# Kernel tuning notes

Measured on AMD Instinct MI355X. Metric: run time of the kernel, lower is better.

## Reference

```python
import jax, jax.numpy as jnp
import numpy as np

N, E = 50000, 800000
ND, ED, H, L = 128, 32, 128, 4


def _mlp2(x, w1, b1, w2, b2):
    return jax.nn.relu(x @ w1 + b1) @ w2 + b2


def _layer_norm(x, g, b, eps=1e-5):
    m = jnp.mean(x, axis=-1, keepdims=True)
    v = jnp.var(x, axis=-1, keepdims=True)
    return (x - m) * jax.lax.rsqrt(v + eps) * g + b


def setup_inputs() -> dict:
    key = jax.random.key(0)
    ks = iter(jax.random.split(key, 40))
    r = lambda *s: jax.random.normal(next(ks), s, jnp.float32) * 0.05
    return dict(
        x=r(N, ND),
        edge_attr=r(E, ED),
        h_prev=r(N, H),
        enc_w1=r(ND, H), enc_b1=jnp.zeros((H,), jnp.float32),
        enc_w2=r(H, H), enc_b2=jnp.zeros((H,), jnp.float32),
        et_w1=r(L, 2 * H + ED, H), et_b1=jnp.zeros((L, H), jnp.float32),
        et_w2=r(L, H, H), et_b2=jnp.zeros((L, H), jnp.float32),
        msg_w1=r(L, H, H), msg_b1=jnp.zeros((L, H), jnp.float32),
        msg_w2=r(L, H, H), msg_b2=jnp.zeros((L, H), jnp.float32),
        upd_w1=r(L, 2 * H, H), upd_b1=jnp.zeros((L, H), jnp.float32),
        upd_w2=r(L, H, H), upd_b2=jnp.zeros((L, H), jnp.float32),
        ln_g=jnp.ones((H,), jnp.float32), ln_b=jnp.zeros((H,), jnp.float32),
        gru_wih=r(3 * H, H), gru_whh=r(3 * H, H),
        gru_bih=jnp.zeros((3 * H,), jnp.float32),
        gru_bhh=jnp.zeros((3 * H,), jnp.float32),
        edge_index=jax.random.randint(next(ks), (2, E), 0, N, jnp.int32),
    )


def reference(x, edge_attr, h_prev,
              enc_w1, enc_b1, enc_w2, enc_b2,
              et_w1, et_b1, et_w2, et_b2,
              msg_w1, msg_b1, msg_w2, msg_b2,
              upd_w1, upd_b1, upd_w2, upd_b2,
              ln_g, ln_b,
              gru_wih, gru_whh, gru_bih, gru_bhh,
              edge_index):
    src, dst = edge_index[0], edge_index[1]  # PyG: x_j = x[src], x_i = x[dst]
    n_nodes = x.shape[0]
    h = _mlp2(x, enc_w1, enc_b1, enc_w2, enc_b2)  # [N, H]
    for l in range(et_w1.shape[0]):
        x_i = h[dst]                                  # [E, H] gather (target)
        x_j = h[src]                                  # [E, H] gather (source)
        e_in = jnp.concatenate([x_i, x_j, edge_attr], axis=-1)  # [E, 2H+ED]
        e_emb = _mlp2(e_in, et_w1[l], et_b1[l], et_w2[l], et_b2[l])
        msg = _mlp2(e_emb, msg_w1[l], msg_b1[l], msg_w2[l], msg_b2[l])
        aggr = jax.ops.segment_sum(msg, dst, num_segments=n_nodes)  # [N, H]
        h_new = _mlp2(jnp.concatenate([h, aggr], axis=-1),
                      upd_w1[l], upd_b1[l], upd_w2[l], upd_b2[l])
        h = _layer_norm(h + h_new, ln_g, ln_b)
    # GRUCell(input=h, hidden=h_prev), torch semantics
    gi = h @ gru_wih.T + gru_bih          # [N, 3H]
    gh = h_prev @ gru_whh.T + gru_bhh     # [N, 3H]
    i_r, i_z, i_n = jnp.split(gi, 3, axis=-1)
    h_r, h_z, h_n = jnp.split(gh, 3, axis=-1)
    r = jax.nn.sigmoid(i_r + h_r)
    z = jax.nn.sigmoid(i_z + h_z)
    n = jnp.tanh(i_n + r * h_n)
    return (1.0 - z) * n + z * h_prev
```

## Files before the change

kernel.cpp:

```cpp
#include <hip/hip_runtime.h>
#include <hip/hip_bf16.h>
#include <cstdint>

#define NN 50000
#define NE 800000

typedef _Float16 f16;
typedef f16 f16x8 __attribute__((ext_vector_type(8)));
typedef f16 f16x4 __attribute__((ext_vector_type(4)));
typedef float f32x4 __attribute__((ext_vector_type(4)));

#define TB_STR 136

__global__ void hist_kernel(const int* __restrict__ edst, int* __restrict__ deg) {
  int e = blockIdx.x * 256 + threadIdx.x;
  if (e < NE) atomicAdd(&deg[edst[e]], 1);
}

__global__ void scan_kernel(const int* __restrict__ deg, int* __restrict__ offs, int n) {
  __shared__ int tmp[256];
  __shared__ int carry;
  const int tid = threadIdx.x;
  if (tid == 0) carry = 0;
  __syncthreads();
  for (int base = 0; base < n; base += 1024) {
    int v[4]; int s = 0;
#pragma unroll
    for (int j = 0; j < 4; ++j) {
      int idx = base + tid * 4 + j;
      v[j] = (idx < n) ? deg[idx] : 0;
      s += v[j];
    }
    tmp[tid] = s;
    __syncthreads();
    for (int ofs = 1; ofs < 256; ofs <<= 1) {
      int t = (tid >= ofs) ? tmp[tid - ofs] : 0;
      __syncthreads();
      tmp[tid] += t;
      __syncthreads();
    }
    int excl = carry + tmp[tid] - s;
#pragma unroll
    for (int j = 0; j < 4; ++j) {
      int idx = base + tid * 4 + j;
      if (idx < n) offs[idx] = excl;
      excl += v[j];
    }
    __syncthreads();
    if (tid == 255) carry += tmp[255];
    __syncthreads();
  }
  if (tid == 0) offs[n] = carry;
}

__global__ void copy_cursor_kernel(const int* __restrict__ offs, int* __restrict__ cursor) {
  int i = blockIdx.x * 256 + threadIdx.x;
  if (i < NN) cursor[i] = offs[i];
}

__global__ void fill_kernel(const int* __restrict__ edst, int* __restrict__ cursor,
                            int* __restrict__ eord) {
  int e = blockIdx.x * 256 + threadIdx.x;
  if (e < NE) {
    int p = atomicAdd(&cursor[edst[e]], 1);
    eord[p] = e;
  }
}

__global__ void permute_kernel(const int* __restrict__ eord,
                               const int* __restrict__ esrc,
                               const int* __restrict__ edst,
                               const float* __restrict__ ea,
                               int* __restrict__ dstp, int* __restrict__ esp,
                               f16* __restrict__ ea16p) {
  int i = blockIdx.x * 256 + threadIdx.x;
  if (i >= NE) return;
  int e = eord[i];
  dstp[i] = edst[e];
  esp[i] = esrc[e];
  const float* sp = ea + (size_t)e * 32;
  f16* dp = ea16p + (size_t)i * 32;
#pragma unroll
  for (int j = 0; j < 4; ++j) {
    float4 u0 = *(const float4*)(sp + j * 8), u1 = *(const float4*)(sp + j * 8 + 4);
    f16x8 v = {(f16)u0.x, (f16)u0.y, (f16)u0.z, (f16)u0.w,
               (f16)u1.x, (f16)u1.y, (f16)u1.z, (f16)u1.w};
    *(f16x8*)(dp + j * 8) = v;
  }
}

__global__ void w23_kernel(const float* __restrict__ et_w2,
                           const float* __restrict__ et_b2,
                           const float* __restrict__ msg_w1,
                           const float* __restrict__ msg_b1,
                           float* __restrict__ w23, float* __restrict__ b23) {
  const int l = blockIdx.x >> 3, cc = blockIdx.x & 7;
  const float* W2 = et_w2 + (size_t)l * 16384;
  const float* W3 = msg_w1 + (size_t)l * 16384;
  __shared__ float w3s[128][17];
  const int tid = threadIdx.x;
#pragma unroll
  for (int it = 0; it < 8; ++it) {
    int f = tid + it * 256;
    int m = f >> 4, n = f & 15;
    w3s[m][n] = W3[m * 128 + cc * 16 + n];
  }
  __syncthreads();
  const int k = tid >> 1, nh = (tid & 1) * 8;
  float s[8] = {};
  for (int m = 0; m < 128; ++m) {
    float w2v = W2[k * 128 + m];
#pragma unroll
    for (int j = 0; j < 8; ++j) s[j] = fmaf(w2v, w3s[m][nh + j], s[j]);
  }
#pragma unroll
  for (int j = 0; j < 8; ++j)
    w23[(size_t)l * 16384 + k * 128 + cc * 16 + nh + j] = s[j];
  if (k == 0) {
    float sb[8] = {};
    for (int m = 0; m < 128; ++m) {
      float b2v = et_b2[l * 128 + m];
#pragma unroll
      for (int j = 0; j < 8; ++j) sb[j] = fmaf(b2v, w3s[m][nh + j], sb[j]);
    }
#pragma unroll
    for (int j = 0; j < 8; ++j)
      b23[l * 128 + cc * 16 + nh + j] = sb[j] + msg_b1[l * 128 + cc * 16 + nh + j];
  }
}

__global__ void pack_w_kernel(const float* __restrict__ et_w1,
                              const float* __restrict__ w23,
                              const float* __restrict__ msg_w2,
                              f16* __restrict__ wpack) {
  int idx = blockIdx.x * 256 + threadIdx.x;
  if (idx >= 4 * 69632) return;
  int l = idx / 69632;
  int rem = idx - l * 69632;
  int unit = rem >> 9;
  int e = rem & 511;
  int ln = e >> 3, i = e & 7;
  const float* src;
  int ul;
  if (unit < 72)       { src = et_w1  + (size_t)l * 288 * 128; ul = unit; }
  else if (unit < 104) { src = w23    + (size_t)l * 16384;     ul = unit - 72; }
  else                 { src = msg_w2 + (size_t)l * 16384;     ul = unit - 104; }
  int kc = ul >> 3, ct = ul & 7;
  int k = kc * 32 + (ln >> 4) * 8 + i;
  int col = ct * 16 + (ln & 15);
  wpack[idx] = (f16)src[k * 128 + col];
}

__global__ void pack_upd_kernel(const float* __restrict__ upd_w1,
                                const float* __restrict__ upd_w2,
                                f16* __restrict__ wpu) {
  int idx = blockIdx.x * 256 + threadIdx.x;
  if (idx >= 4 * 96 * 512) return;
  int l = idx / (96 * 512);
  int rem = idx - l * (96 * 512);
  int unit = rem >> 9, e = rem & 511, ln = e >> 3, i = e & 7;
  const float* src;
  int ul;
  if (unit < 64) { src = upd_w1 + (size_t)l * 256 * 128; ul = unit; }
  else           { src = upd_w2 + (size_t)l * 128 * 128; ul = unit - 64; }
  int kc = ul >> 3, ct = ul & 7;
  int k = kc * 32 + (ln >> 4) * 8 + i;
  int col = ct * 16 + (ln & 15);
  wpu[idx] = (f16)src[k * 128 + col];
}

__global__ void pack_gru_kernel(const float* __restrict__ wih,
                                const float* __restrict__ whh,
                                const float* __restrict__ bih,
                                const float* __restrict__ bhh,
                                f16* __restrict__ wg, float* __restrict__ brz) {
  int idx = blockIdx.x * 256 + threadIdx.x;
  if (idx < 256) brz[idx] = bih[idx] + bhh[idx];
  if (idx >= 192 * 512) return;
  int unit = idx >> 9, e = idx & 511, ln = e >> 3, i = e & 7;
  int krow = (ln >> 4) * 8 + i;
  int cl16 = ln & 15;
  f16 val;
  if (unit < 128) {
    int kc = unit >> 4, ctg = unit & 15;
    int k = kc * 32 + krow;
    int col = ctg * 16 + cl16;
    float w = (k < 128) ? wih[col * 128 + k] : whh[col * 128 + (k - 128)];
    val = (f16)w;
  } else if (unit < 160) {
    int ul = unit - 128;
    int k = (ul >> 3) * 32 + krow;
    int col = (ul & 7) * 16 + cl16;
    val = (f16)wih[(256 + col) * 128 + k];
  } else {
    int ul = unit - 160;
    int k = (ul >> 3) * 32 + krow;
    int col = (ul & 7) * 16 + cl16;
    val = (f16)whh[(256 + col) * 128 + k];
  }
  wg[idx] = val;
}

__global__ void pack_enc_kernel(const float* __restrict__ w1,
                                const float* __restrict__ w2,
                                f16* __restrict__ wpenc) {
  int idx = blockIdx.x * 256 + threadIdx.x;
  if (idx >= 64 * 512) return;
  int unit = idx >> 9, e = idx & 511, ln = e >> 3, i = e & 7;
  const float* src = (unit < 32) ? w1 : w2;
  int ul = unit & 31;
  int k = (ul >> 3) * 32 + (ln >> 4) * 8 + i;
  int col = (ul & 7) * 16 + (ln & 15);
  wpenc[idx] = (f16)src[k * 128 + col];
}

__global__ void cvt_x_kernel(const float* __restrict__ x, f16* __restrict__ x16) {
  int idx = blockIdx.x * 256 + threadIdx.x;
  if (idx >= NN * 16) return;
  const float* sp = x + (size_t)idx * 8;
  float4 u0 = *(const float4*)sp, u1 = *(const float4*)(sp + 4);
  f16x8 v = {(f16)u0.x, (f16)u0.y, (f16)u0.z, (f16)u0.w,
             (f16)u1.x, (f16)u1.y, (f16)u1.z, (f16)u1.w};
  *(f16x8*)(x16 + (size_t)idx * 8) = v;
}

#define EDGE_ACC_INIT(BIAS)                                                    \
  _Pragma("unroll") for (int ct = 0; ct < 4; ++ct) {                           \
    float bv_ = (BIAS)[wc * 64 + ct * 16 + cl];                                \
    acc[0][ct] = (f32x4){bv_, bv_, bv_, bv_};                                  \
    acc[1][ct] = acc[0][ct];                                                   \
  }

#define EDGE_MFMA_KC(A0, A1, UNIT)                                             \
  _Pragma("unroll") for (int ct = 0; ct < 4; ++ct) {                           \
    f16x8 b_ = *(const f16x8*)&wp[(size_t)(((UNIT) + wc * 4 + ct) * 64 + lane) * 8]; \
    acc[0][ct] = __builtin_amdgcn_mfma_f32_16x16x32_f16(A0, b_, acc[0][ct], 0, 0, 0); \
    acc[1][ct] = __builtin_amdgcn_mfma_f32_16x16x32_f16(A1, b_, acc[1][ct], 0, 0, 0); \
  }

#define EDGE_GEMM_LDS(APTR, UNIT0, BIAS)                                       \
  {                                                                            \
    EDGE_ACC_INIT(BIAS);                                                       \
    _Pragma("unroll") for (int kc = 0; kc < 4; ++kc) {                         \
      f16x8 a0_ = *(const f16x8*)&(APTR)[(wr * 32 + cl) * TB_STR + kc * 32 + kh * 8]; \
      f16x8 a1_ = *(const f16x8*)&(APTR)[(wr * 32 + 16 + cl) * TB_STR + kc * 32 + kh * 8]; \
      EDGE_MFMA_KC(a0_, a1_, (UNIT0) + kc * 8);                                \
    }                                                                          \
  }

#define EDGE_STORE(DST, RELU)                                                  \
  _Pragma("unroll") for (int rt = 0; rt < 2; ++rt)                             \
    _Pragma("unroll") for (int ct = 0; ct < 4; ++ct)                           \
      _Pragma("unroll") for (int i = 0; i < 4; ++i) {                          \
        float v_ = acc[rt][ct][i];                                             \
        if (RELU) v_ = fmaxf(v_, 0.f);                                         \
        (DST)[(wr * 32 + rt * 16 + kh * 4 + i) * TB_STR + wc * 64 + ct * 16 + cl] = (f16)v_; \
      }

__global__ __launch_bounds__(256, 6)
void edge_mfma_kernel(const f16* __restrict__ h16, const f16* __restrict__ ea16p,
                      const int* __restrict__ esp, const int* __restrict__ dstp,
                      const f16* __restrict__ wp,
                      const float* __restrict__ b1, const float* __restrict__ b23,
                      const float* __restrict__ b4,
                      float* __restrict__ aggrf) {
  __shared__ f16 buf[64 * TB_STR];
  __shared__ int eidx[128];
  const int tid = threadIdx.x;
  const int lane = tid & 63;
  const int wv = tid >> 6;
  const int wr = wv >> 1, wc = wv & 1;
  const int cl = lane & 15;
  const int kh = lane >> 4;
  const int e0 = blockIdx.x * 64;
  if (tid < 64) eidx[tid] = dstp[e0 + tid];
  else if (tid < 128) eidx[tid] = esp[e0 + tid - 64];
  __syncthreads();

  const int r0 = wr * 32 + cl, r1 = r0 + 16;
  const f16* pd0 = h16 + (size_t)eidx[r0] * 128 + kh * 8;
  const f16* pd1 = h16 + (size_t)eidx[r1] * 128 + kh * 8;
  const f16* ps0 = h16 + (size_t)eidx[64 + r0] * 128 + kh * 8;
  const f16* ps1 = h16 + (size_t)eidx[64 + r1] * 128 + kh * 8;
  const f16* pe0 = ea16p + (size_t)(e0 + r0) * 32 + kh * 8;
  const f16* pe1 = ea16p + (size_t)(e0 + r1) * 32 + kh * 8;

  f32x4 acc[2][4];
  EDGE_ACC_INIT(b1);
#pragma unroll
  for (int kc = 0; kc < 4; ++kc) {
    f16x8 a0_ = *(const f16x8*)(pd0 + kc * 32);
    f16x8 a1_ = *(const f16x8*)(pd1 + kc * 32);
    EDGE_MFMA_KC(a0_, a1_, kc * 8);
  }
#pragma unroll
  for (int kc = 4; kc < 8; ++kc) {
    f16x8 a0_ = *(const f16x8*)(ps0 + (kc - 4) * 32);
    f16x8 a1_ = *(const f16x8*)(ps1 + (kc - 4) * 32);
    EDGE_MFMA_KC(a0_, a1_, kc * 8);
  }
  {
    f16x8 a0_ = *(const f16x8*)pe0;
    f16x8 a1_ = *(const f16x8*)pe1;
    EDGE_MFMA_KC(a0_, a1_, 64);
  }
  EDGE_STORE(buf, 1);
  __syncthreads();
  EDGE_GEMM_LDS(buf, 72, b23);
  __syncthreads();
  EDGE_STORE(buf, 1);
  __syncthreads();
  EDGE_GEMM_LDS(buf, 104, b4);
  __syncthreads();
  EDGE_STORE(buf, 0);
  __syncthreads();
  {
    const int c = tid & 127;
    const int rbeg = (tid >> 7) * 32;
    float sum = 0.f;
    int cur = eidx[rbeg];
    bool openL = true;
    for (int r = rbeg; r < rbeg + 32; ++r) {
      sum += (float)buf[r * TB_STR + c];
      bool last = (r == rbeg + 31);
      int nxt = last ? -1 : eidx[r + 1];
      if (last || nxt != cur) {
        float* ap = aggrf + (size_t)cur * 128 + c;
        if (openL || last) unsafeAtomicAdd(ap, sum);
        else *ap = sum;
        sum = 0.f; cur = nxt; openL = false;
      }
    }
  }
}

__global__ __launch_bounds__(256, 4)
void encoder_mfma_kernel(const f16* __restrict__ x16, const f16* __restrict__ wp,
                         const float* __restrict__ b1, const float* __restrict__ b2,
                         f16* __restrict__ h16out) {
  __shared__ f16 buf[64 * TB_STR];
  const int tid = threadIdx.x;
  const int lane = tid & 63;
  const int wv = tid >> 6;
  const int wr = wv >> 1, wc = wv & 1;
  const int cl = lane & 15;
  const int kh = lane >> 4;
  const int r0 = blockIdx.x * 64;
  const int gr0 = min(r0 + wr * 32 + cl, NN - 1);
  const int gr1 = min(r0 + wr * 32 + 16 + cl, NN - 1);
  const f16* px0 = x16 + (size_t)gr0 * 128 + kh * 8;
  const f16* px1 = x16 + (size_t)gr1 * 128 + kh * 8;
  f32x4 acc[2][4];
  EDGE_ACC_INIT(b1);
#pragma unroll
  for (int kc = 0; kc < 4; ++kc) {
    f16x8 a0_ = *(const f16x8*)(px0 + kc * 32);
    f16x8 a1_ = *(const f16x8*)(px1 + kc * 32);
    EDGE_MFMA_KC(a0_, a1_, kc * 8);
  }
  EDGE_STORE(buf, 1);
  __syncthreads();
  EDGE_GEMM_LDS(buf, 32, b2);
  __syncthreads();
  EDGE_STORE(buf, 0);
  __syncthreads();
#pragma unroll
  for (int it = 0; it < 4; ++it) {
    int f = tid + it * 256;
    int row = f >> 4, c8 = f & 15;
    int grow = r0 + row;
    if (grow < NN) {
      f16x8 v = *(const f16x8*)&buf[row * TB_STR + c8 * 8];
      *(f16x8*)(h16out + (size_t)grow * 128 + c8 * 8) = v;
    }
  }
}

__global__ __launch_bounds__(256, 2)
void gru_mfma_kernel(const f16* __restrict__ h16, const float* __restrict__ hprev,
                     const f16* __restrict__ wg, const float* __restrict__ brz,
                     const float* __restrict__ bih, const float* __restrict__ bhh,
                     float* __restrict__ out) {
  __shared__ f16 ac[64 * 264];
  __shared__ f16 rz[64 * 264];
  const int tid = threadIdx.x;
  const int lane = tid & 63;
  const int wv = tid >> 6;
  const int wr = wv >> 1, wc = wv & 1;
  const int cl = lane & 15;
  const int kh = lane >> 4;
  const int r0 = blockIdx.x * 64;
#pragma unroll
  for (int it = 0; it < 8; ++it) {
    int f = tid + it * 256;
    int row = f >> 5, c8 = f & 31;
    int grow = r0 + row;
    f16x8 v = {};
    if (grow < NN) {
      if (c8 < 16) {
        v = *(const f16x8*)(h16 + (size_t)grow * 128 + c8 * 8);
      } else {
        const float* sp = hprev + (size_t)grow * 128 + (c8 - 16) * 8;
        float4 u0 = *(const float4*)sp, u1 = *(const float4*)(sp + 4);
        v = (f16x8){(f16)u0.x, (f16)u0.y, (f16)u0.z, (f16)u0.w,
                    (f16)u1.x, (f16)u1.y, (f16)u1.z, (f16)u1.w};
      }
    }
    *(f16x8*)&ac[row * 264 + c8 * 8] = v;
  }
  __syncthreads();
  {
    f32x4 az[4][4];
#pragma unroll
    for (int ct = 0; ct < 4; ++ct) {
      float bv = brz[wv * 64 + ct * 16 + cl];
#pragma unroll
      for (int rt = 0; rt < 4; ++rt) az[rt][ct] = (f32x4){bv, bv, bv, bv};
    }
#pragma unroll
    for (int kc = 0; kc < 8; ++kc) {
      f16x8 a_[4];
#pragma unroll
      for (int rt = 0; rt < 4; ++rt)
        a_[rt] = *(const f16x8*)&ac[(rt * 16 + cl) * 264 + kc * 32 + kh * 8];
#pragma unroll
      for (int ct = 0; ct < 4; ++ct) {
        f16x8 b_ = *(const f16x8*)&wg[(size_t)((kc * 16 + wv * 4 + ct) * 64 + lane) * 8];
#pragma unroll
        for (int rt = 0; rt < 4; ++rt)
          az[rt][ct] = __builtin_amdgcn_mfma_f32_16x16x32_f16(a_[rt], b_, az[rt][ct], 0, 0, 0);
      }
    }
#pragma unroll
    for (int rt = 0; rt < 4; ++rt)
#pragma unroll
      for (int ct = 0; ct < 4; ++ct)
#pragma unroll
        for (int i = 0; i < 4; ++i) {
          float sg = 1.f / (1.f + __expf(-az[rt][ct][i]));
          rz[(rt * 16 + kh * 4 + i) * 264 + wv * 64 + ct * 16 + cl] = (f16)sg;
        }
  }
  __syncthreads();
  f32x4 ai_[2][4], ah_[2][4];
#pragma unroll
  for (int ct = 0; ct < 4; ++ct) {
    float bi = bih[256 + wc * 64 + ct * 16 + cl];
    float bh = bhh[256 + wc * 64 + ct * 16 + cl];
    ai_[0][ct] = (f32x4){bi, bi, bi, bi}; ai_[1][ct] = ai_[0][ct];
    ah_[0][ct] = (f32x4){bh, bh, bh, bh}; ah_[1][ct] = ah_[0][ct];
  }
#pragma unroll
  for (int kc = 0; kc < 4; ++kc) {
    f16x8 a0 = *(const f16x8*)&ac[(wr * 32 + cl) * 264 + kc * 32 + kh * 8];
    f16x8 a1 = *(const f16x8*)&ac[(wr * 32 + 16 + cl) * 264 + kc * 32 + kh * 8];
    f16x8 p0 = *(const f16x8*)&ac[(wr * 32 + cl) * 264 + 128 + kc * 32 + kh * 8];
    f16x8 p1 = *(const f16x8*)&ac[(wr * 32 + 16 + cl) * 264 + 128 + kc * 32 + kh * 8];
#pragma unroll
    for (int ct = 0; ct < 4; ++ct) {
      f16x8 bi_ = *(const f16x8*)&wg[(size_t)(((128 + kc * 8 + wc * 4 + ct)) * 64 + lane) * 8];
      f16x8 bh_ = *(const f16x8*)&wg[(size_t)(((160 + kc * 8 + wc * 4 + ct)) * 64 + lane) * 8];
      ai_[0][ct] = __builtin_amdgcn_mfma_f32_16x16x32_f16(a0, bi_, ai_[0][ct], 0, 0, 0);
      ai_[1][ct] = __builtin_amdgcn_mfma_f32_16x16x32_f16(a1, bi_, ai_[1][ct], 0, 0, 0);
      ah_[0][ct] = __builtin_amdgcn_mfma_f32_16x16x32_f16(p0, bh_, ah_[0][ct], 0, 0, 0);
      ah_[1][ct] = __builtin_amdgcn_mfma_f32_16x16x32_f16(p1, bh_, ah_[1][ct], 0, 0, 0);
    }
  }
#pragma unroll
  for (int rt = 0; rt < 2; ++rt)
#pragma unroll
    for (int ct = 0; ct < 4; ++ct)
#pragma unroll
      for (int i = 0; i < 4; ++i) {
        int row = wr * 32 + rt * 16 + kh * 4 + i;
        int col = wc * 64 + ct * 16 + cl;
        int grow = r0 + row;
        if (grow < NN) {
          float r_ = (float)rz[row * 264 + col];
          float z_ = (float)rz[row * 264 + 128 + col];
          float n_ = tanhf(ai_[rt][ct][i] + r_ * ah_[rt][ct][i]);
          float hpv = (float)ac[row * 264 + 128 + col];
          out[(size_t)grow * 128 + col] = (1.f - z_) * n_ + z_ * hpv;
        }
      }
}

#define MFMA_T(APTR, ASTR, ASWZ, NKC, UNIT0, BIAS)                             \
  {                                                                            \
    _Pragma("unroll") for (int nt = 0; nt < 2; ++nt) {                         \
      f32x4 bv_ = *(const f32x4*)((BIAS) + wv * 32 + nt * 16 + kh * 4);        \
      _Pragma("unroll") for (int et = 0; et < 4; ++et) acc[nt][et] = bv_;      \
    }                                                                          \
    _Pragma("unroll 2") for (int kc = 0; kc < (NKC); ++kc) {                   \
      f16x8 wfr_[2];                                                           \
      _Pragma("unroll") for (int nt = 0; nt < 2; ++nt)                         \
        wfr_[nt] = *(const f16x8*)&wp[(size_t)(((UNIT0) + kc * 8 + wv * 2 + nt) * 64 + lane) * 8]; \
      _Pragma("unroll") for (int et = 0; et < 4; ++et) {                       \
        int r_ = et * 16 + cl;                                                 \
        int idx_ = r_ * (ASTR) + kc * 32 + kh * 8;                             \
        if (ASWZ) idx_ ^= ((r_ & 7) << 3);                                     \
        f16x8 efr_ = *(const f16x8*)&(APTR)[idx_];                             \
        _Pragma("unroll") for (int nt = 0; nt < 2; ++nt)                       \
          acc[nt][et] = __builtin_amdgcn_mfma_f32_16x16x32_f16(wfr_[nt], efr_, acc[nt][et], 0, 0, 0); \
      }                                                                        \
    }                                                                          \
  }

#define STORE_T(DPTR, RELU)                                                    \
  _Pragma("unroll") for (int nt = 0; nt < 2; ++nt)                             \
    _Pragma("unroll") for (int et = 0; et < 4; ++et) {                         \
      float v0_ = acc[nt][et][0], v1_ = acc[nt][et][1],                        \
            v2_ = acc[nt][et][2], v3_ = acc[nt][et][3];                        \
      if (RELU) { v0_ = fmaxf(v0_, 0.f); v1_ = fmaxf(v1_, 0.f);                \
                  v2_ = fmaxf(v2_, 0.f); v3_ = fmaxf(v3_, 0.f); }              \
      int r_ = et * 16 + cl;                                                   \
      int idx_ = (r_ * 128 + wv * 32 + nt * 16 + kh * 4) ^ ((r_ & 7) << 3);    \
      *(f16x4*)&(DPTR)[idx_] = (f16x4){(f16)v0_, (f16)v1_, (f16)v2_, (f16)v3_};\
    }

__global__ __launch_bounds__(256, 2)
void update_mfma_kernel(const f16* __restrict__ h16, const float* __restrict__ aggr,
                        const f16* __restrict__ wp,
                        const float* __restrict__ b1, const float* __restrict__ b2,
                        const float* __restrict__ lng, const float* __restrict__ lnb,
                        f16* __restrict__ h16out) {
  __shared__ f16 ua[64 * 264];
  __shared__ f16 tb[64 * 128];
  __shared__ f16 emb[64 * 128];
  const int tid = threadIdx.x;
  const int lane = tid & 63;
  const int wv = tid >> 6;
  const int cl = lane & 15;
  const int kh = lane >> 4;
  const int r0 = blockIdx.x * 64;
#pragma unroll
  for (int it = 0; it < 8; ++it) {
    int f = tid + it * 256;
    int row = f >> 5, c8 = f & 31;
    int grow = r0 + row;
    f16x8 v = {};
    if (grow < NN) {
      if (c8 < 16) {
        v = *(const f16x8*)(h16 + (size_t)grow * 128 + c8 * 8);
      } else {
        const float* sp = aggr + (size_t)grow * 128 + (c8 - 16) * 8;
        float4 u0 = *(const float4*)sp, u1 = *(const float4*)(sp + 4);
        v = (f16x8){(f16)u0.x, (f16)u0.y, (f16)u0.z, (f16)u0.w,
                    (f16)u1.x, (f16)u1.y, (f16)u1.z, (f16)u1.w};
      }
    }
    *(f16x8*)&ua[row * 264 + c8 * 8] = v;
  }
  __syncthreads();
  f32x4 acc[2][4];
  MFMA_T(ua, 264, 0, 8, 0, b1);
  STORE_T(tb, 1);
  __syncthreads();
  MFMA_T(tb, 128, 1, 4, 64, b2);
  STORE_T(emb, 0);
  __syncthreads();
  {
    const int row = tid >> 2, q = tid & 3;
    const int grow = r0 + row;
    float y[32];
    float s = 0.f, ss = 0.f;
#pragma unroll
    for (int j = 0; j < 4; ++j) {
      int col = q * 32 + j * 8;
      int ei = (row * 128 + col) ^ ((row & 7) << 3);
      f16x8 ev = *(const f16x8*)&emb[ei];
      f16x8 rv = *(const f16x8*)&ua[row * 264 + col];
#pragma unroll
      for (int e = 0; e < 8; ++e) {
        float t = (float)ev[e] + (float)rv[e];
        y[j * 8 + e] = t; s += t; ss += t * t;
      }
    }
    s += __shfl_xor(s, 1);  s += __shfl_xor(s, 2);
    ss += __shfl_xor(ss, 1); ss += __shfl_xor(ss, 2);
    float mean = s * (1.f / 128.f);
    float var = ss * (1.f / 128.f) - mean * mean;
    float rstd = rsqrtf(var + 1e-5f);
    if (grow < NN) {
#pragma unroll
      for (int j = 0; j < 4; ++j) {
        int col = q * 32 + j * 8;
        const float4 g0 = *(const float4*)(lng + col), g1 = *(const float4*)(lng + col + 4);
        const float4 q0 = *(const float4*)(lnb + col), q1 = *(const float4*)(lnb + col + 4);
        float gv[8] = {g0.x, g0.y, g0.z, g0.w, g1.x, g1.y, g1.z, g1.w};
        float bv[8] = {q0.x, q0.y, q0.z, q0.w, q1.x, q1.y, q1.z, q1.w};
        f16x8 o;
#pragma unroll
        for (int e = 0; e < 8; ++e)
          o[e] = (f16)((y[j * 8 + e] - mean) * rstd * gv[e] + bv[e]);
        *(f16x8*)(h16out + (size_t)grow * 128 + col) = o;
      }
    }
  }
}

extern "C" void kernel_launch(void* const* d_in, const int* in_sizes, int n_in,
                              void* d_out, int out_size, void* d_ws, size_t ws_size,
                              hipStream_t stream) {
  (void)in_sizes; (void)n_in; (void)out_size; (void)ws_size;
  const float* x         = (const float*)d_in[0];
  const float* edge_attr = (const float*)d_in[1];
  const float* h_prev    = (const float*)d_in[2];
  const float* enc_w1    = (const float*)d_in[3];
  const float* enc_b1    = (const float*)d_in[4];
  const float* enc_w2    = (const float*)d_in[5];
  const float* enc_b2    = (const float*)d_in[6];
  const float* et_w1     = (const float*)d_in[7];
  const float* et_b1     = (const float*)d_in[8];
  const float* et_w2     = (const float*)d_in[9];
  const float* et_b2     = (const float*)d_in[10];
  const float* msg_w1    = (const float*)d_in[11];
  const float* msg_b1    = (const float*)d_in[12];
  const float* msg_w2    = (const float*)d_in[13];
  const float* msg_b2    = (const float*)d_in[14];
  const float* upd_w1    = (const float*)d_in[15];
  const float* upd_b1    = (const float*)d_in[16];
  const float* upd_w2    = (const float*)d_in[17];
  const float* upd_b2    = (const float*)d_in[18];
  const float* ln_g      = (const float*)d_in[19];
  const float* ln_b      = (const float*)d_in[20];
  const float* gru_wih   = (const float*)d_in[21];
  const float* gru_whh   = (const float*)d_in[22];
  const float* gru_bih   = (const float*)d_in[23];
  const float* gru_bhh   = (const float*)d_in[24];
  const int* edge_index  = (const int*)d_in[25];
  const int* esrc = edge_index;
  const int* edst = edge_index + NE;

  float* ws    = (float*)d_ws;
  float* aggrf = ws;
  float* wreg  = ws + (size_t)NN * 128;
  f16*   wg    = (f16*)wreg;
  float* brz   = wreg + 49152;
  f16*   wpenc = (f16*)(brz + 256);
  f16*   h16a  = (f16*)(wreg + 98304);
  f16*   h16b  = h16a + (size_t)NN * 128;
  f16*   wpe   = h16b + (size_t)NN * 128;
  f16*   wpu   = wpe + 4 * 69632;
  f16*   ea16p = wpu + 4 * 96 * 512;
  float* w23f  = (float*)(ea16p + (size_t)NE * 32);
  float* b23f  = w23f + 4 * 16384;

  int* iout   = (int*)d_out;
  int* deg    = iout;
  int* offs   = iout + 51200;
  int* cursor = iout + 102400;
  int* eord   = iout + 153600;
  int* dstp   = iout + 153600 + NE;
  int* esp    = iout + 153600 + 2 * NE;
  f16* x16    = (f16*)(iout + 2600000);

  hipMemsetAsync(deg, 0, NN * sizeof(int), stream);
  hist_kernel<<<(NE + 255) / 256, 256, 0, stream>>>(edst, deg);
  scan_kernel<<<1, 256, 0, stream>>>(deg, offs, NN);
  copy_cursor_kernel<<<(NN + 255) / 256, 256, 0, stream>>>(offs, cursor);
  fill_kernel<<<(NE + 255) / 256, 256, 0, stream>>>(edst, cursor, eord);
  permute_kernel<<<(NE + 255) / 256, 256, 0, stream>>>(eord, esrc, edst, edge_attr,
                                                       dstp, esp, ea16p);

  w23_kernel<<<32, 256, 0, stream>>>(et_w2, et_b2, msg_w1, msg_b1, w23f, b23f);
  pack_w_kernel<<<(4 * 69632 + 255) / 256, 256, 0, stream>>>(et_w1, w23f, msg_w2, wpe);
  pack_upd_kernel<<<(4 * 96 * 512 + 255) / 256, 256, 0, stream>>>(upd_w1, upd_w2, wpu);
  pack_gru_kernel<<<(192 * 512 + 255) / 256, 256, 0, stream>>>(gru_wih, gru_whh,
                                                               gru_bih, gru_bhh, wg, brz);
  pack_enc_kernel<<<(64 * 512 + 255) / 256, 256, 0, stream>>>(enc_w1, enc_w2, wpenc);
  cvt_x_kernel<<<(NN * 16 + 255) / 256, 256, 0, stream>>>(x, x16);
  encoder_mfma_kernel<<<(NN + 63) / 64, 256, 0, stream>>>(x16, wpenc, enc_b1, enc_b2, h16a);

  f16* hc = h16a;
  f16* hn = h16b;
  for (int l = 0; l < 4; ++l) {
    hipMemsetAsync(aggrf, 0, (size_t)NN * 128 * sizeof(float), stream);
    edge_mfma_kernel<<<NE / 64, 256, 0, stream>>>(
        hc, ea16p, esp, dstp,
        wpe + (size_t)l * 69632,
        et_b1 + l * 128, b23f + l * 128, msg_b2 + l * 128,
        aggrf);
    update_mfma_kernel<<<(NN + 63) / 64, 256, 0, stream>>>(
        hc, aggrf,
        wpu + (size_t)l * 96 * 512,
        upd_b1 + l * 128, upd_b2 + l * 128,
        ln_g, ln_b, hn);
    f16* t = hc; hc = hn; hn = t;
  }
  gru_mfma_kernel<<<(NN + 63) / 64, 256, 0, stream>>>(hc, h_prev, wg, brz,
                                                      gru_bih, gru_bhh, (float*)d_out);
}
```

Baseline: 1.168 ms.

## Rework edge MLP kernel to transposed MFMA tiling with swizzled LDS buffer

The edge kernel now uses the transposed MFMA scheme already used by the update kernel. Weights are the A operand and edges the B operand, and each wave covers 32 output columns across all 64 edges rather than a 32x64 quadrant. Intermediate activations go into an XOR-swizzled 64x128 LDS buffer written with packed f16x4 stores, replacing the padded stride-136 buffer and its scalar stores. Each gathered h row is now loaded by all four waves instead of two, while each wave loads half as many weight fragments. Launch bounds drop from 6 to 5 blocks per SM, likely to give the compiler more registers.

```diff
diff --git a/kernel.cpp b/kernel.cpp
--- a/kernel.cpp
+++ b/kernel.cpp
@@ -224,267 +224,6 @@
   *(f16x8*)(x16 + (size_t)idx * 8) = v;
 }
 
-#define EDGE_ACC_INIT(BIAS)                                                    \
-  _Pragma("unroll") for (int ct = 0; ct < 4; ++ct) {                           \
-    float bv_ = (BIAS)[wc * 64 + ct * 16 + cl];                                \
-    acc[0][ct] = (f32x4){bv_, bv_, bv_, bv_};                                  \
-    acc[1][ct] = acc[0][ct];                                                   \
-  }
-
-#define EDGE_MFMA_KC(A0, A1, UNIT)                                             \
-  _Pragma("unroll") for (int ct = 0; ct < 4; ++ct) {                           \
-    f16x8 b_ = *(const f16x8*)&wp[(size_t)(((UNIT) + wc * 4 + ct) * 64 + lane) * 8]; \
-    acc[0][ct] = __builtin_amdgcn_mfma_f32_16x16x32_f16(A0, b_, acc[0][ct], 0, 0, 0); \
-    acc[1][ct] = __builtin_amdgcn_mfma_f32_16x16x32_f16(A1, b_, acc[1][ct], 0, 0, 0); \
-  }
-
-#define EDGE_GEMM_LDS(APTR, UNIT0, BIAS)                                       \
-  {                                                                            \
-    EDGE_ACC_INIT(BIAS);                                                       \
-    _Pragma("unroll") for (int kc = 0; kc < 4; ++kc) {                         \
-      f16x8 a0_ = *(const f16x8*)&(APTR)[(wr * 32 + cl) * TB_STR + kc * 32 + kh * 8]; \
-      f16x8 a1_ = *(const f16x8*)&(APTR)[(wr * 32 + 16 + cl) * TB_STR + kc * 32 + kh * 8]; \
-      EDGE_MFMA_KC(a0_, a1_, (UNIT0) + kc * 8);                                \
-    }                                                                          \
-  }
-
-#define EDGE_STORE(DST, RELU)                                                  \
-  _Pragma("unroll") for (int rt = 0; rt < 2; ++rt)                             \
-    _Pragma("unroll") for (int ct = 0; ct < 4; ++ct)                           \
-      _Pragma("unroll") for (int i = 0; i < 4; ++i) {                          \
-        float v_ = acc[rt][ct][i];                                             \
-        if (RELU) v_ = fmaxf(v_, 0.f);                                         \
-        (DST)[(wr * 32 + rt * 16 + kh * 4 + i) * TB_STR + wc * 64 + ct * 16 + cl] = (f16)v_; \
-      }
-
-__global__ __launch_bounds__(256, 6)
-void edge_mfma_kernel(const f16* __restrict__ h16, const f16* __restrict__ ea16p,
-                      const int* __restrict__ esp, const int* __restrict__ dstp,
-                      const f16* __restrict__ wp,
-                      const float* __restrict__ b1, const float* __restrict__ b23,
-                      const float* __restrict__ b4,
-                      float* __restrict__ aggrf) {
-  __shared__ f16 buf[64 * TB_STR];
-  __shared__ int eidx[128];
-  const int tid = threadIdx.x;
-  const int lane = tid & 63;
-  const int wv = tid >> 6;
-  const int wr = wv >> 1, wc = wv & 1;
-  const int cl = lane & 15;
-  const int kh = lane >> 4;
-  const int e0 = blockIdx.x * 64;
-  if (tid < 64) eidx[tid] = dstp[e0 + tid];
-  else if (tid < 128) eidx[tid] = esp[e0 + tid - 64];
-  __syncthreads();
-
-  const int r0 = wr * 32 + cl, r1 = r0 + 16;
-  const f16* pd0 = h16 + (size_t)eidx[r0] * 128 + kh * 8;
-  const f16* pd1 = h16 + (size_t)eidx[r1] * 128 + kh * 8;
-  const f16* ps0 = h16 + (size_t)eidx[64 + r0] * 128 + kh * 8;
-  const f16* ps1 = h16 + (size_t)eidx[64 + r1] * 128 + kh * 8;
-  const f16* pe0 = ea16p + (size_t)(e0 + r0) * 32 + kh * 8;
-  const f16* pe1 = ea16p + (size_t)(e0 + r1) * 32 + kh * 8;
-
-  f32x4 acc[2][4];
-  EDGE_ACC_INIT(b1);
-#pragma unroll
-  for (int kc = 0; kc < 4; ++kc) {
-    f16x8 a0_ = *(const f16x8*)(pd0 + kc * 32);
-    f16x8 a1_ = *(const f16x8*)(pd1 + kc * 32);
-    EDGE_MFMA_KC(a0_, a1_, kc * 8);
-  }
-#pragma unroll
-  for (int kc = 4; kc < 8; ++kc) {
-    f16x8 a0_ = *(const f16x8*)(ps0 + (kc - 4) * 32);
-    f16x8 a1_ = *(const f16x8*)(ps1 + (kc - 4) * 32);
-    EDGE_MFMA_KC(a0_, a1_, kc * 8);
-  }
-  {
-    f16x8 a0_ = *(const f16x8*)pe0;
-    f16x8 a1_ = *(const f16x8*)pe1;
-    EDGE_MFMA_KC(a0_, a1_, 64);
-  }
-  EDGE_STORE(buf, 1);
-  __syncthreads();
-  EDGE_GEMM_LDS(buf, 72, b23);
-  __syncthreads();
-  EDGE_STORE(buf, 1);
-  __syncthreads();
-  EDGE_GEMM_LDS(buf, 104, b4);
-  __syncthreads();
-  EDGE_STORE(buf, 0);
-  __syncthreads();
-  {
-    const int c = tid & 127;
-    const int rbeg = (tid >> 7) * 32;
-    float sum = 0.f;
-    int cur = eidx[rbeg];
-    bool openL = true;
-    for (int r = rbeg; r < rbeg + 32; ++r) {
-      sum += (float)buf[r * TB_STR + c];
-      bool last = (r == rbeg + 31);
-      int nxt = last ? -1 : eidx[r + 1];
-      if (last || nxt != cur) {
-        float* ap = aggrf + (size_t)cur * 128 + c;
-        if (openL || last) unsafeAtomicAdd(ap, sum);
-        else *ap = sum;
-        sum = 0.f; cur = nxt; openL = false;
-      }
-    }
-  }
-}
-
-__global__ __launch_bounds__(256, 4)
-void encoder_mfma_kernel(const f16* __restrict__ x16, const f16* __restrict__ wp,
-                         const float* __restrict__ b1, const float* __restrict__ b2,
-                         f16* __restrict__ h16out) {
-  __shared__ f16 buf[64 * TB_STR];
-  const int tid = threadIdx.x;
-  const int lane = tid & 63;
-  const int wv = tid >> 6;
-  const int wr = wv >> 1, wc = wv & 1;
-  const int cl = lane & 15;
-  const int kh = lane >> 4;
-  const int r0 = blockIdx.x * 64;
-  const int gr0 = min(r0 + wr * 32 + cl, NN - 1);
-  const int gr1 = min(r0 + wr * 32 + 16 + cl, NN - 1);
-  const f16* px0 = x16 + (size_t)gr0 * 128 + kh * 8;
-  const f16* px1 = x16 + (size_t)gr1 * 128 + kh * 8;
-  f32x4 acc[2][4];
-  EDGE_ACC_INIT(b1);
-#pragma unroll
-  for (int kc = 0; kc < 4; ++kc) {
-    f16x8 a0_ = *(const f16x8*)(px0 + kc * 32);
-    f16x8 a1_ = *(const f16x8*)(px1 + kc * 32);
-    EDGE_MFMA_KC(a0_, a1_, kc * 8);
-  }
-  EDGE_STORE(buf, 1);
-  __syncthreads();
-  EDGE_GEMM_LDS(buf, 32, b2);
-  __syncthreads();
-  EDGE_STORE(buf, 0);
-  __syncthreads();
-#pragma unroll
-  for (int it = 0; it < 4; ++it) {
-    int f = tid + it * 256;
-    int row = f >> 4, c8 = f & 15;
-    int grow = r0 + row;
-    if (grow < NN) {
-      f16x8 v = *(const f16x8*)&buf[row * TB_STR + c8 * 8];
-      *(f16x8*)(h16out + (size_t)grow * 128 + c8 * 8) = v;
-    }
-  }
-}
-
-__global__ __launch_bounds__(256, 2)
-void gru_mfma_kernel(const f16* __restrict__ h16, const float* __restrict__ hprev,
-                     const f16* __restrict__ wg, const float* __restrict__ brz,
-                     const float* __restrict__ bih, const float* __restrict__ bhh,
-                     float* __restrict__ out) {
-  __shared__ f16 ac[64 * 264];
-  __shared__ f16 rz[64 * 264];
-  const int tid = threadIdx.x;
-  const int lane = tid & 63;
-  const int wv = tid >> 6;
-  const int wr = wv >> 1, wc = wv & 1;
-  const int cl = lane & 15;
-  const int kh = lane >> 4;
-  const int r0 = blockIdx.x * 64;
-#pragma unroll
-  for (int it = 0; it < 8; ++it) {
-    int f = tid + it * 256;
-    int row = f >> 5, c8 = f & 31;
-    int grow = r0 + row;
-    f16x8 v = {};
-    if (grow < NN) {
-      if (c8 < 16) {
-        v = *(const f16x8*)(h16 + (size_t)grow * 128 + c8 * 8);
-      } else {
-        const float* sp = hprev + (size_t)grow * 128 + (c8 - 16) * 8;
-        float4 u0 = *(const float4*)sp, u1 = *(const float4*)(sp + 4);
-        v = (f16x8){(f16)u0.x, (f16)u0.y, (f16)u0.z, (f16)u0.w,
-                    (f16)u1.x, (f16)u1.y, (f16)u1.z, (f16)u1.w};
-      }
-    }
-    *(f16x8*)&ac[row * 264 + c8 * 8] = v;
-  }
-  __syncthreads();
-  {
-    f32x4 az[4][4];
-#pragma unroll
-    for (int ct = 0; ct < 4; ++ct) {
-      float bv = brz[wv * 64 + ct * 16 + cl];
-#pragma unroll
-      for (int rt = 0; rt < 4; ++rt) az[rt][ct] = (f32x4){bv, bv, bv, bv};
-    }
-#pragma unroll
-    for (int kc = 0; kc < 8; ++kc) {
-      f16x8 a_[4];
-#pragma unroll
-      for (int rt = 0; rt < 4; ++rt)
-        a_[rt] = *(const f16x8*)&ac[(rt * 16 + cl) * 264 + kc * 32 + kh * 8];
-#pragma unroll
-      for (int ct = 0; ct < 4; ++ct) {
-        f16x8 b_ = *(const f16x8*)&wg[(size_t)((kc * 16 + wv * 4 + ct) * 64 + lane) * 8];
-#pragma unroll
-        for (int rt = 0; rt < 4; ++rt)
-          az[rt][ct] = __builtin_amdgcn_mfma_f32_16x16x32_f16(a_[rt], b_, az[rt][ct], 0, 0, 0);
-      }
-    }
-#pragma unroll
-    for (int rt = 0; rt < 4; ++rt)
-#pragma unroll
-      for (int ct = 0; ct < 4; ++ct)
-#pragma unroll
-        for (int i = 0; i < 4; ++i) {
-          float sg = 1.f / (1.f + __expf(-az[rt][ct][i]));
-          rz[(rt * 16 + kh * 4 + i) * 264 + wv * 64 + ct * 16 + cl] = (f16)sg;
-        }
-  }
-  __syncthreads();
-  f32x4 ai_[2][4], ah_[2][4];
-#pragma unroll
-  for (int ct = 0; ct < 4; ++ct) {
-    float bi = bih[256 + wc * 64 + ct * 16 + cl];
-    float bh = bhh[256 + wc * 64 + ct * 16 + cl];
-    ai_[0][ct] = (f32x4){bi, bi, bi, bi}; ai_[1][ct] = ai_[0][ct];
-    ah_[0][ct] = (f32x4){bh, bh, bh, bh}; ah_[1][ct] = ah_[0][ct];
-  }
-#pragma unroll
-  for (int kc = 0; kc < 4; ++kc) {
-    f16x8 a0 = *(const f16x8*)&ac[(wr * 32 + cl) * 264 + kc * 32 + kh * 8];
-    f16x8 a1 = *(const f16x8*)&ac[(wr * 32 + 16 + cl) * 264 + kc * 32 + kh * 8];
-    f16x8 p0 = *(const f16x8*)&ac[(wr * 32 + cl) * 264 + 128 + kc * 32 + kh * 8];
-    f16x8 p1 = *(const f16x8*)&ac[(wr * 32 + 16 + cl) * 264 + 128 + kc * 32 + kh * 8];
-#pragma unroll
-    for (int ct = 0; ct < 4; ++ct) {
-      f16x8 bi_ = *(const f16x8*)&wg[(size_t)(((128 + kc * 8 + wc * 4 + ct)) * 64 + lane) * 8];
-      f16x8 bh_ = *(const f16x8*)&wg[(size_t)(((160 + kc * 8 + wc * 4 + ct)) * 64 + lane) * 8];
-      ai_[0][ct] = __builtin_amdgcn_mfma_f32_16x16x32_f16(a0, bi_, ai_[0][ct], 0, 0, 0);
-      ai_[1][ct] = __builtin_amdgcn_mfma_f32_16x16x32_f16(a1, bi_, ai_[1][ct], 0, 0, 0);
-      ah_[0][ct] = __builtin_amdgcn_mfma_f32_16x16x32_f16(p0, bh_, ah_[0][ct], 0, 0, 0);
-      ah_[1][ct] = __builtin_amdgcn_mfma_f32_16x16x32_f16(p1, bh_, ah_[1][ct], 0, 0, 0);
-    }
-  }
-#pragma unroll
-  for (int rt = 0; rt < 2; ++rt)
-#pragma unroll
-    for (int ct = 0; ct < 4; ++ct)
-#pragma unroll
-      for (int i = 0; i < 4; ++i) {
-        int row = wr * 32 + rt * 16 + kh * 4 + i;
-        int col = wc * 64 + ct * 16 + cl;
-        int grow = r0 + row;
-        if (grow < NN) {
-          float r_ = (float)rz[row * 264 + col];
-          float z_ = (float)rz[row * 264 + 128 + col];
-          float n_ = tanhf(ai_[rt][ct][i] + r_ * ah_[rt][ct][i]);
-          float hpv = (float)ac[row * 264 + 128 + col];
-          out[(size_t)grow * 128 + col] = (1.f - z_) * n_ + z_ * hpv;
-        }
-      }
-}
-
 #define MFMA_T(APTR, ASTR, ASWZ, NKC, UNIT0, BIAS)                             \
   {                                                                            \
     _Pragma("unroll") for (int nt = 0; nt < 2; ++nt) {                         \
@@ -517,6 +256,294 @@
       int idx_ = (r_ * 128 + wv * 32 + nt * 16 + kh * 4) ^ ((r_ & 7) << 3);    \
       *(f16x4*)&(DPTR)[idx_] = (f16x4){(f16)v0_, (f16)v1_, (f16)v2_, (f16)v3_};\
     }
+
+__global__ __launch_bounds__(256, 5)
+void edge_mfma_kernel(const f16* __restrict__ h16, const f16* __restrict__ ea16p,
+                      const int* __restrict__ esp, const int* __restrict__ dstp,
+                      const f16* __restrict__ wp,
+                      const float* __restrict__ b1, const float* __restrict__ b23,
+                      const float* __restrict__ b4,
+                      float* __restrict__ aggrf) {
+  __shared__ f16 buf[64 * 128];
+  __shared__ int eidx[128];
+  const int tid = threadIdx.x;
+  const int lane = tid & 63;
+  const int wv = tid >> 6;
+  const int cl = lane & 15;
+  const int kh = lane >> 4;
+  const int e0 = blockIdx.x * 64;
+  if (tid < 64) eidx[tid] = dstp[e0 + tid];
+  else if (tid < 128) eidx[tid] = esp[e0 + tid - 64];
+  __syncthreads();
+
+  int er[4], es[4];
+#pragma unroll
+  for (int et = 0; et < 4; ++et) {
+    er[et] = eidx[et * 16 + cl];
+    es[et] = eidx[64 + et * 16 + cl];
+  }
+
+  f32x4 acc[2][4];
+#pragma unroll
+  for (int nt = 0; nt < 2; ++nt) {
+    f32x4 bv_ = *(const f32x4*)(b1 + wv * 32 + nt * 16 + kh * 4);
+#pragma unroll
+    for (int et = 0; et < 4; ++et) acc[nt][et] = bv_;
+  }
+#pragma unroll
+  for (int kc = 0; kc < 4; ++kc) {
+    f16x8 wfr_[2];
+#pragma unroll
+    for (int nt = 0; nt < 2; ++nt)
+      wfr_[nt] = *(const f16x8*)&wp[(size_t)((kc * 8 + wv * 2 + nt) * 64 + lane) * 8];
+#pragma unroll
+    for (int et = 0; et < 4; ++et) {
+      f16x8 efr_ = *(const f16x8*)(h16 + (size_t)er[et] * 128 + kc * 32 + kh * 8);
+#pragma unroll
+      for (int nt = 0; nt < 2; ++nt)
+        acc[nt][et] = __builtin_amdgcn_mfma_f32_16x16x32_f16(wfr_[nt], efr_, acc[nt][et], 0, 0, 0);
+    }
+  }
+#pragma unroll
+  for (int kc = 4; kc < 8; ++kc) {
+    f16x8 wfr_[2];
+#pragma unroll
+    for (int nt = 0; nt < 2; ++nt)
+      wfr_[nt] = *(const f16x8*)&wp[(size_t)((kc * 8 + wv * 2 + nt) * 64 + lane) * 8];
+#pragma unroll
+    for (int et = 0; et < 4; ++et) {
+      f16x8 efr_ = *(const f16x8*)(h16 + (size_t)es[et] * 128 + (kc - 4) * 32 + kh * 8);
+#pragma unroll
+      for (int nt = 0; nt < 2; ++nt)
+        acc[nt][et] = __builtin_amdgcn_mfma_f32_16x16x32_f16(wfr_[nt], efr_, acc[nt][et], 0, 0, 0);
+    }
+  }
+  {
+    f16x8 wfr_[2];
+#pragma unroll
+    for (int nt = 0; nt < 2; ++nt)
+      wfr_[nt] = *(const f16x8*)&wp[(size_t)((64 + wv * 2 + nt) * 64 + lane) * 8];
+#pragma unroll
+    for (int et = 0; et < 4; ++et) {
+      f16x8 efr_ = *(const f16x8*)(ea16p + (size_t)(e0 + et * 16 + cl) * 32 + kh * 8);
+#pragma unroll
+      for (int nt = 0; nt < 2; ++nt)
+        acc[nt][et] = __builtin_amdgcn_mfma_f32_16x16x32_f16(wfr_[nt], efr_, acc[nt][et], 0, 0, 0);
+    }
+  }
+  STORE_T(buf, 1);
+  __syncthreads();
+  MFMA_T(buf, 128, 1, 4, 72, b23);
+  __syncthreads();
+  STORE_T(buf, 1);
+  __syncthreads();
+  MFMA_T(buf, 128, 1, 4, 104, b4);
+  __syncthreads();
+  STORE_T(buf, 0);
+  __syncthreads();
+  {
+    const int c = tid & 127;
+    const int rbeg = (tid >> 7) * 32;
+    float sum = 0.f;
+    int cur = eidx[rbeg];
+    bool openL = true;
+    for (int r = rbeg; r < rbeg + 32; ++r) {
+      sum += (float)buf[(r * 128 + c) ^ ((r & 7) << 3)];
+      bool last = (r == rbeg + 31);
+      int nxt = last ? -1 : eidx[r + 1];
+      if (last || nxt != cur) {
+        float* ap = aggrf + (size_t)cur * 128 + c;
+        if (openL || last) unsafeAtomicAdd(ap, sum);
+        else *ap = sum;
+        sum = 0.f; cur = nxt; openL = false;
+      }
+    }
+  }
+}
+
+#define EDGE_ACC_INIT(BIAS)                                                    \
+  _Pragma("unroll") for (int ct = 0; ct < 4; ++ct) {                           \
+    float bv_ = (BIAS)[wc * 64 + ct * 16 + cl];                                \
+    acc[0][ct] = (f32x4){bv_, bv_, bv_, bv_};                                  \
+    acc[1][ct] = acc[0][ct];                                                   \
+  }
+
+#define EDGE_MFMA_KC(A0, A1, UNIT)                                             \
+  _Pragma("unroll") for (int ct = 0; ct < 4; ++ct) {                           \
+    f16x8 b_ = *(const f16x8*)&wp[(size_t)(((UNIT) + wc * 4 + ct) * 64 + lane) * 8]; \
+    acc[0][ct] = __builtin_amdgcn_mfma_f32_16x16x32_f16(A0, b_, acc[0][ct], 0, 0, 0); \
+    acc[1][ct] = __builtin_amdgcn_mfma_f32_16x16x32_f16(A1, b_, acc[1][ct], 0, 0, 0); \
+  }
+
+#define EDGE_GEMM_LDS(APTR, UNIT0, BIAS)                                       \
+  {                                                                            \
+    EDGE_ACC_INIT(BIAS);                                                       \
+    _Pragma("unroll") for (int kc = 0; kc < 4; ++kc) {                         \
+      f16x8 a0_ = *(const f16x8*)&(APTR)[(wr * 32 + cl) * TB_STR + kc * 32 + kh * 8]; \
+      f16x8 a1_ = *(const f16x8*)&(APTR)[(wr * 32 + 16 + cl) * TB_STR + kc * 32 + kh * 8]; \
+      EDGE_MFMA_KC(a0_, a1_, (UNIT0) + kc * 8);                                \
+    }                                                                          \
+  }
+
+#define EDGE_STORE(DST, RELU)                                                  \
+  _Pragma("unroll") for (int rt = 0; rt < 2; ++rt)                             \
+    _Pragma("unroll") for (int ct = 0; ct < 4; ++ct)                           \
+      _Pragma("unroll") for (int i = 0; i < 4; ++i) {                          \
+        float v_ = acc[rt][ct][i];                                             \
+        if (RELU) v_ = fmaxf(v_, 0.f);                                         \
+        (DST)[(wr * 32 + rt * 16 + kh * 4 + i) * TB_STR + wc * 64 + ct * 16 + cl] = (f16)v_; \
+      }
+
+__global__ __launch_bounds__(256, 4)
+void encoder_mfma_kernel(const f16* __restrict__ x16, const f16* __restrict__ wp,
+                         const float* __restrict__ b1, const float* __restrict__ b2,
+                         f16* __restrict__ h16out) {
+  __shared__ f16 buf[64 * TB_STR];
+  const int tid = threadIdx.x;
+  const int lane = tid & 63;
+  const int wv = tid >> 6;
+  const int wr = wv >> 1, wc = wv & 1;
+  const int cl = lane & 15;
+  const int kh = lane >> 4;
+  const int r0 = blockIdx.x * 64;
+  const int gr0 = min(r0 + wr * 32 + cl, NN - 1);
+  const int gr1 = min(r0 + wr * 32 + 16 + cl, NN - 1);
+  const f16* px0 = x16 + (size_t)gr0 * 128 + kh * 8;
+  const f16* px1 = x16 + (size_t)gr1 * 128 + kh * 8;
+  f32x4 acc[2][4];
+  EDGE_ACC_INIT(b1);
+#pragma unroll
+  for (int kc = 0; kc < 4; ++kc) {
+    f16x8 a0_ = *(const f16x8*)(px0 + kc * 32);
+    f16x8 a1_ = *(const f16x8*)(px1 + kc * 32);
+    EDGE_MFMA_KC(a0_, a1_, kc * 8);
+  }
+  EDGE_STORE(buf, 1);
+  __syncthreads();
+  EDGE_GEMM_LDS(buf, 32, b2);
+  __syncthreads();
+  EDGE_STORE(buf, 0);
+  __syncthreads();
+#pragma unroll
+  for (int it = 0; it < 4; ++it) {
+    int f = tid + it * 256;
+    int row = f >> 4, c8 = f & 15;
+    int grow = r0 + row;
+    if (grow < NN) {
+      f16x8 v = *(const f16x8*)&buf[row * TB_STR + c8 * 8];
+      *(f16x8*)(h16out + (size_t)grow * 128 + c8 * 8) = v;
+    }
+  }
+}
+
+__global__ __launch_bounds__(256, 2)
+void gru_mfma_kernel(const f16* __restrict__ h16, const float* __restrict__ hprev,
+                     const f16* __restrict__ wg, const float* __restrict__ brz,
+                     const float* __restrict__ bih, const float* __restrict__ bhh,
+                     float* __restrict__ out) {
+  __shared__ f16 ac[64 * 264];
+  __shared__ f16 rz[64 * 264];
+  const int tid = threadIdx.x;
+  const int lane = tid & 63;
+  const int wv = tid >> 6;
+  const int wr = wv >> 1, wc = wv & 1;
+  const int cl = lane & 15;
+  const int kh = lane >> 4;
+  const int r0 = blockIdx.x * 64;
+#pragma unroll
+  for (int it = 0; it < 8; ++it) {
+    int f = tid + it * 256;
+    int row = f >> 5, c8 = f & 31;
+    int grow = r0 + row;
+    f16x8 v = {};
+    if (grow < NN) {
+      if (c8 < 16) {
+        v = *(const f16x8*)(h16 + (size_t)grow * 128 + c8 * 8);
+      } else {
+        const float* sp = hprev + (size_t)grow * 128 + (c8 - 16) * 8;
+        float4 u0 = *(const float4*)sp, u1 = *(const float4*)(sp + 4);
+        v = (f16x8){(f16)u0.x, (f16)u0.y, (f16)u0.z, (f16)u0.w,
+                    (f16)u1.x, (f16)u1.y, (f16)u1.z, (f16)u1.w};
+      }
+    }
+    *(f16x8*)&ac[row * 264 + c8 * 8] = v;
+  }
+  __syncthreads();
+  {
+    f32x4 az[4][4];
+#pragma unroll
+    for (int ct = 0; ct < 4; ++ct) {
+      float bv = brz[wv * 64 + ct * 16 + cl];
+#pragma unroll
+      for (int rt = 0; rt < 4; ++rt) az[rt][ct] = (f32x4){bv, bv, bv, bv};
+    }
+#pragma unroll
+    for (int kc = 0; kc < 8; ++kc) {
+      f16x8 a_[4];
+#pragma unroll
+      for (int rt = 0; rt < 4; ++rt)
+        a_[rt] = *(const f16x8*)&ac[(rt * 16 + cl) * 264 + kc * 32 + kh * 8];
+#pragma unroll
+      for (int ct = 0; ct < 4; ++ct) {
+        f16x8 b_ = *(const f16x8*)&wg[(size_t)((kc * 16 + wv * 4 + ct) * 64 + lane) * 8];
+#pragma unroll
+        for (int rt = 0; rt < 4; ++rt)
+          az[rt][ct] = __builtin_amdgcn_mfma_f32_16x16x32_f16(a_[rt], b_, az[rt][ct], 0, 0, 0);
+      }
+    }
+#pragma unroll
+    for (int rt = 0; rt < 4; ++rt)
+#pragma unroll
+      for (int ct = 0; ct < 4; ++ct)
+#pragma unroll
+        for (int i = 0; i < 4; ++i) {
+          float sg = 1.f / (1.f + __expf(-az[rt][ct][i]));
+          rz[(rt * 16 + kh * 4 + i) * 264 + wv * 64 + ct * 16 + cl] = (f16)sg;
+        }
+  }
+  __syncthreads();
+  f32x4 ai_[2][4], ah_[2][4];
+#pragma unroll
+  for (int ct = 0; ct < 4; ++ct) {
+    float bi = bih[256 + wc * 64 + ct * 16 + cl];
+    float bh = bhh[256 + wc * 64 + ct * 16 + cl];
+    ai_[0][ct] = (f32x4){bi, bi, bi, bi}; ai_[1][ct] = ai_[0][ct];
+    ah_[0][ct] = (f32x4){bh, bh, bh, bh}; ah_[1][ct] = ah_[0][ct];
+  }
+#pragma unroll
+  for (int kc = 0; kc < 4; ++kc) {
+    f16x8 a0 = *(const f16x8*)&ac[(wr * 32 + cl) * 264 + kc * 32 + kh * 8];
+    f16x8 a1 = *(const f16x8*)&ac[(wr * 32 + 16 + cl) * 264 + kc * 32 + kh * 8];
+    f16x8 p0 = *(const f16x8*)&ac[(wr * 32 + cl) * 264 + 128 + kc * 32 + kh * 8];
+    f16x8 p1 = *(const f16x8*)&ac[(wr * 32 + 16 + cl) * 264 + 128 + kc * 32 + kh * 8];
+#pragma unroll
+    for (int ct = 0; ct < 4; ++ct) {
+      f16x8 bi_ = *(const f16x8*)&wg[(size_t)(((128 + kc * 8 + wc * 4 + ct)) * 64 + lane) * 8];
+      f16x8 bh_ = *(const f16x8*)&wg[(size_t)(((160 + kc * 8 + wc * 4 + ct)) * 64 + lane) * 8];
+      ai_[0][ct] = __builtin_amdgcn_mfma_f32_16x16x32_f16(a0, bi_, ai_[0][ct], 0, 0, 0);
+      ai_[1][ct] = __builtin_amdgcn_mfma_f32_16x16x32_f16(a1, bi_, ai_[1][ct], 0, 0, 0);
+      ah_[0][ct] = __builtin_amdgcn_mfma_f32_16x16x32_f16(p0, bh_, ah_[0][ct], 0, 0, 0);
+      ah_[1][ct] = __builtin_amdgcn_mfma_f32_16x16x32_f16(p1, bh_, ah_[1][ct], 0, 0, 0);
+    }
+  }
+#pragma unroll
+  for (int rt = 0; rt < 2; ++rt)
+#pragma unroll
+    for (int ct = 0; ct < 4; ++ct)
+#pragma unroll
+      for (int i = 0; i < 4; ++i) {
+        int row = wr * 32 + rt * 16 + kh * 4 + i;
+        int col = wc * 64 + ct * 16 + cl;
+        int grow = r0 + row;
+        if (grow < NN) {
+          float r_ = (float)rz[row * 264 + col];
+          float z_ = (float)rz[row * 264 + 128 + col];
+          float n_ = tanhf(ai_[rt][ct][i] + r_ * ah_[rt][ct][i]);
+          float hpv = (float)ac[row * 264 + 128 + col];
+          out[(size_t)grow * 128 + col] = (1.f - z_) * n_ + z_ * hpv;
+        }
+      }
+}
 
 __global__ __launch_bounds__(256, 2)
 void update_mfma_kernel(const f16* __restrict__ h16, const float* __restrict__ aggr,
```

Result: slower. 1.280 ms (+9.6%).
